# Performance work log

Measured on AMD Instinct MI355X. Metric: run time of the kernel, lower is better.

The kernel has to match this reference:

```python
import jax, jax.numpy as jnp
import numpy as np
import math

B, L, D = 32, 512, 256
H, DK, DV = 8, 32, 32
DFF = 2048
CONCAT = D * H * DV + D  # 65792


def setup_inputs() -> dict:
    key = jax.random.key(0)
    ks = jax.random.split(key, 12)
    s = 0.02
    return {
        "input_emb": jax.random.normal(ks[0], (B, L, D), jnp.float32),
        "emb_self_attn_mask": jax.random.bernoulli(ks[1], 0.1, (B, L, L)),
        "input_mask": jax.random.bernoulli(ks[2], 0.9, (B, L)).astype(jnp.int32),
        "W_Q": jax.random.normal(ks[3], (D, H * DK), jnp.float32) * s,
        "W_K": jax.random.normal(ks[4], (D, H * DK), jnp.float32) * s,
        "W_V": jax.random.normal(ks[5], (D, H * DV), jnp.float32) * s,
        "fc1_w": jax.random.normal(ks[6], (CONCAT, DFF), jnp.float32) * s,
        "fc1_b": jnp.zeros((DFF,), jnp.float32),
        "fc2_w": jax.random.normal(ks[7], (DFF, DFF), jnp.float32) * s,
        "fc2_b": jnp.zeros((DFF,), jnp.float32),
        "fc3_w": jax.random.normal(ks[8], (DFF, 1), jnp.float32) * s,
        "fc3_b": jnp.zeros((1,), jnp.float32),
    }


def reference(input_emb, emb_self_attn_mask, input_mask,
              W_Q, W_K, W_V, fc1_w, fc1_b, fc2_w, fc2_b, fc3_w, fc3_b):
    b, l, d = input_emb.shape
    # multi-head attention (hand-rolled SDPA)
    Q = (input_emb @ W_Q).reshape(b, l, H, DK).transpose(0, 2, 1, 3)  # [B,H,L,dk]
    K = (input_emb @ W_K).reshape(b, l, H, DK).transpose(0, 2, 1, 3)
    V = (input_emb @ W_V).reshape(b, l, H, DV).transpose(0, 2, 1, 3)
    scores = jnp.einsum("bhqd,bhkd->bhqk", Q, K) / math.sqrt(DK)
    scores = jnp.where(emb_self_attn_mask[:, None, :, :], -1e9, scores)
    attn = jax.nn.softmax(scores, axis=-1)
    context = jnp.einsum("bhqk,bhkd->bhqd", attn, V)
    context = context.transpose(0, 2, 1, 3).reshape(b, l, H * DV)  # [B,L,H*dv]
    # masked softmax pooling over the sequence dimension
    mask_exp = input_mask[:, :, None]  # [B,L,1]
    ctx_masked = jnp.where(mask_exp == 0, -1e9, context)
    weights = jax.nn.softmax(ctx_masked, axis=1)               # [B,L,H*dv]
    pooled = jnp.einsum("bld,blc->bdc", input_emb, weights)    # [B,D,H*dv]
    pooled_flat = pooled.reshape(b, -1)
    # masked mean pooling
    fmask = mask_exp.astype(input_emb.dtype)
    lengths = jnp.maximum(jnp.sum(input_mask, axis=1, keepdims=True), 1).astype(input_emb.dtype)
    avg_emb = jnp.sum(input_emb * fmask, axis=1) / lengths     # [B,D]
    x = jnp.concatenate([pooled_flat, avg_emb], axis=1)        # [B,CONCAT]
    h1 = jax.nn.relu(x @ fc1_w + fc1_b)
    h2 = jax.nn.relu(h1 @ fc2_w + fc2_b)
    out = h2 @ fc3_w + fc3_b                                    # [B,1]
    return (out, attn)
```

## Files before the change

kernel.cpp:

```cpp
#include <hip/hip_runtime.h>
#include <hip/hip_bf16.h>
#include <cstdint>

namespace {
constexpr int B  = 32;
constexpr int L  = 512;
constexpr int D  = 256;
constexpr int H  = 8;
constexpr int DV = 32;
constexpr int DFF = 2048;
constexpr int CONCAT = D * H * DV + D;
constexpr int BH = B * H;
}

typedef __attribute__((ext_vector_type(8))) short bf16x8;
typedef __attribute__((ext_vector_type(4))) float f32x4;

static __device__ __forceinline__ unsigned short f2bf_bits(float x) {
    __hip_bfloat16 h = __float2bfloat16(x);
    return *reinterpret_cast<unsigned short*>(&h);
}
static __device__ __forceinline__ float bf2f(short u) {
    unsigned int x = ((unsigned int)(unsigned short)u) << 16;
    union { unsigned int u; float f; } c; c.u = x; return c.f;
}
static __device__ __forceinline__ bf16x8 pack8(const float* v) {
    bf16x8 r;
#pragma unroll
    for (int j = 0; j < 8; ++j) r[j] = (short)f2bf_bits(v[j]);
    return r;
}

__global__ __launch_bounds__(256) void maskpack(const int* __restrict__ amask,
                                                unsigned int* __restrict__ mb) {
    const int t = threadIdx.x;
    const size_t gid = (size_t)blockIdx.x * 256 + t;
    int v = amask[gid];
    unsigned long long bal = __ballot(v != 0);
    if ((t & 63) == 0) *reinterpret_cast<unsigned long long*>(mb + (gid >> 5)) = bal;
}

__global__ __launch_bounds__(256) void transW(const float* __restrict__ WQ,
                                              const float* __restrict__ WK,
                                              const float* __restrict__ WV,
                                              __hip_bfloat16* __restrict__ WT) {
    const int mat = blockIdx.y;
    const int idx = blockIdx.x * 256 + threadIdx.x;
    const int n = idx >> 8, k = idx & 255;
    const float* W = (mat == 0) ? WQ : (mat == 1) ? WK : WV;
    WT[(size_t)mat * 65536 + idx] = __float2bfloat16(W[(size_t)k * 256 + n]);
}

__global__ __launch_bounds__(256) void embtrans(const float* __restrict__ emb,
                                                __hip_bfloat16* __restrict__ embB,
                                                __hip_bfloat16* __restrict__ embT) {
    const int lc = blockIdx.x;
    const int b  = blockIdx.y;
    const int t = threadIdx.x;
    __shared__ __hip_bfloat16 tile[64][264];
    const int l0 = lc * 64;
#pragma unroll 4
    for (int i = 0; i < 64; ++i) {
        float v = emb[((size_t)b * 512 + l0 + i) * 256 + t];
        __hip_bfloat16 hv = __float2bfloat16(v);
        embB[((size_t)b * 512 + l0 + i) * 256 + t] = hv;
        tile[i][t] = hv;
    }
    __syncthreads();
    __hip_bfloat16* dst = embT + ((size_t)b * 256 + t) * 512 + l0;
#pragma unroll
    for (int i0 = 0; i0 < 64; i0 += 8) {
        bf16x8 v;
#pragma unroll
        for (int j = 0; j < 8; ++j) v[j] = *reinterpret_cast<short*>(&tile[i0 + j][t]);
        *reinterpret_cast<bf16x8*>(dst + i0) = v;
    }
}

__global__ __launch_bounds__(256) void proj_mfma(const __hip_bfloat16* __restrict__ embB,
                                                 const __hip_bfloat16* __restrict__ WT,
                                                 __hip_bfloat16* __restrict__ Qb,
                                                 __hip_bfloat16* __restrict__ Kb,
                                                 __hip_bfloat16* __restrict__ Vt) {
    const int rb = blockIdx.x * 32;
    const int t = threadIdx.x;
    const int w = t >> 6, l = t & 63;
    const int lr = l & 15, lg = l >> 4;

    f32x4 accQ[2][4], accK[2][4], accV[2][4];
#pragma unroll
    for (int m = 0; m < 2; ++m)
#pragma unroll
        for (int n = 0; n < 4; ++n) {
            accQ[m][n] = (f32x4){0.f,0.f,0.f,0.f};
            accK[m][n] = (f32x4){0.f,0.f,0.f,0.f};
            accV[m][n] = (f32x4){0.f,0.f,0.f,0.f};
        }

    for (int kc = 0; kc < 8; ++kc) {
        const int k0 = kc * 32 + lg * 8;
        bf16x8 a0 = *reinterpret_cast<const bf16x8*>(embB + (size_t)(rb + lr) * 256 + k0);
        bf16x8 a1 = *reinterpret_cast<const bf16x8*>(embB + (size_t)(rb + 16 + lr) * 256 + k0);
#pragma unroll
        for (int nt = 0; nt < 4; ++nt) {
            const int col = w * 64 + nt * 16 + lr;
            bf16x8 bq = *reinterpret_cast<const bf16x8*>(WT + (size_t)col * 256 + k0);
            bf16x8 bk = *reinterpret_cast<const bf16x8*>(WT + 65536 + (size_t)col * 256 + k0);
            bf16x8 bv = *reinterpret_cast<const bf16x8*>(WT + 131072 + (size_t)col * 256 + k0);
            accQ[0][nt] = __builtin_amdgcn_mfma_f32_16x16x32_bf16(a0, bq, accQ[0][nt], 0, 0, 0);
            accQ[1][nt] = __builtin_amdgcn_mfma_f32_16x16x32_bf16(a1, bq, accQ[1][nt], 0, 0, 0);
            accK[0][nt] = __builtin_amdgcn_mfma_f32_16x16x32_bf16(a0, bk, accK[0][nt], 0, 0, 0);
            accK[1][nt] = __builtin_amdgcn_mfma_f32_16x16x32_bf16(a1, bk, accK[1][nt], 0, 0, 0);
            accV[0][nt] = __builtin_amdgcn_mfma_f32_16x16x32_bf16(a0, bv, accV[0][nt], 0, 0, 0);
            accV[1][nt] = __builtin_amdgcn_mfma_f32_16x16x32_bf16(a1, bv, accV[1][nt], 0, 0, 0);
        }
    }

    const int b = rb >> 9, l0 = rb & 511;
#pragma unroll
    for (int m = 0; m < 2; ++m)
#pragma unroll
        for (int nt = 0; nt < 4; ++nt) {
            const int n = w * 64 + nt * 16 + lr;
            const int h = n >> 5, d = n & 31;
            const int bh = b * 8 + h;
#pragma unroll
            for (int r = 0; r < 4; ++r) {
                const int ll = l0 + m * 16 + lg * 4 + r;
                Qb[((size_t)bh * 512 + ll) * 32 + d] = __float2bfloat16(accQ[m][nt][r]);
                Kb[((size_t)bh * 512 + ll) * 32 + d] = __float2bfloat16(accK[m][nt][r]);
                Vt[((size_t)bh * 32 + d) * 512 + ll] = __float2bfloat16(accV[m][nt][r]);
            }
        }
}

__global__ __launch_bounds__(256) void attn_mfma(const __hip_bfloat16* __restrict__ Q,
                                                 const __hip_bfloat16* __restrict__ K,
                                                 const __hip_bfloat16* __restrict__ Vt,
                                                 const unsigned int* __restrict__ mb,
                                                 float* __restrict__ attn_out,
                                                 float* __restrict__ ctx) {
    const int qt = blockIdx.x;
    const int bh = blockIdx.y;
    const int b = bh >> 3, h = bh & 7;
    const int t = threadIdx.x;
    const int w = t >> 6, l = t & 63;
    const int lr = l & 15, lg = l >> 4;
    const int q0 = qt * 16;

    __shared__ __hip_bfloat16 Pl[4][16][40];
    __shared__ float rmax[4][16];
    __shared__ float rsum[4][16];
    __shared__ float Ored[4][16][32];

    const float scale = 0.17677669529663687f;

    const bf16x8 aq = *reinterpret_cast<const bf16x8*>(Q + ((size_t)bh * L + q0 + lr) * 32 + lg * 8);
    const __hip_bfloat16* Kbase = K + (size_t)bh * L * 32;

    f32x4 sc[8];
#pragma unroll
    for (int kt = 0; kt < 8; ++kt) {
        bf16x8 bk = *reinterpret_cast<const bf16x8*>(
            Kbase + (size_t)((w * 8 + kt) * 16 + lr) * 32 + lg * 8);
        sc[kt] = __builtin_amdgcn_mfma_f32_16x16x32_bf16(aq, bk, (f32x4){0.f,0.f,0.f,0.f}, 0, 0, 0);
    }

    float tmp[4];
#pragma unroll
    for (int r = 0; r < 4; ++r) {
        const int q = q0 + lg * 4 + r;
        uint4 mw = *reinterpret_cast<const uint4*>(mb + ((size_t)b * L + q) * 16 + w * 4);
        const unsigned int wds[4] = {mw.x, mw.y, mw.z, mw.w};
        float m = -3.4e38f;
#pragma unroll
        for (int kt = 0; kt < 8; ++kt) {
            unsigned bit = (unsigned)lr + ((kt & 1) << 4);
            float s = ((wds[kt >> 1] >> bit) & 1u) ? -1e9f : sc[kt][r] * scale;
            sc[kt][r] = s;
            m = fmaxf(m, s);
        }
        m = fmaxf(m, __shfl_xor(m, 1));
        m = fmaxf(m, __shfl_xor(m, 2));
        m = fmaxf(m, __shfl_xor(m, 4));
        m = fmaxf(m, __shfl_xor(m, 8));
        tmp[r] = m;
    }
    if (lr == 0) {
#pragma unroll
        for (int r = 0; r < 4; ++r) rmax[w][lg * 4 + r] = tmp[r];
    }
    __syncthreads();

#pragma unroll
    for (int r = 0; r < 4; ++r) {
        const int row = lg * 4 + r;
        const float gm = fmaxf(fmaxf(rmax[0][row], rmax[1][row]),
                               fmaxf(rmax[2][row], rmax[3][row]));
        float sum = 0.f;
#pragma unroll
        for (int kt = 0; kt < 8; ++kt) {
            float e = __expf(sc[kt][r] - gm);
            sc[kt][r] = e;
            sum += e;
        }
        sum += __shfl_xor(sum, 1);
        sum += __shfl_xor(sum, 2);
        sum += __shfl_xor(sum, 4);
        sum += __shfl_xor(sum, 8);
        tmp[r] = sum;
    }
    if (lr == 0) {
#pragma unroll
        for (int r = 0; r < 4; ++r) rsum[w][lg * 4 + r] = tmp[r];
    }
    __syncthreads();

    const float my_ri = 1.f / (rsum[0][lr] + rsum[1][lr] + rsum[2][lr] + rsum[3][lr]);

    f32x4 acc0 = {0.f,0.f,0.f,0.f}, acc1 = {0.f,0.f,0.f,0.f};
    const __hip_bfloat16* Vb = Vt + (size_t)bh * 32 * L;
    float* aob = attn_out + ((size_t)bh * L + q0 + lr) * L + w * 128;
#pragma unroll
    for (int cc = 0; cc < 4; ++cc) {
#pragma unroll
        for (int r = 0; r < 4; ++r) {
            Pl[w][lg * 4 + r][lr]      = __float2bfloat16(sc[2*cc  ][r]);
            Pl[w][lg * 4 + r][16 + lr] = __float2bfloat16(sc[2*cc+1][r]);
        }
        __syncthreads();
        bf16x8 ap = *reinterpret_cast<const bf16x8*>(&Pl[w][lr][lg * 8]);
        float4 o0, o1;
        o0.x = bf2f(ap[0]) * my_ri; o0.y = bf2f(ap[1]) * my_ri;
        o0.z = bf2f(ap[2]) * my_ri; o0.w = bf2f(ap[3]) * my_ri;
        o1.x = bf2f(ap[4]) * my_ri; o1.y = bf2f(ap[5]) * my_ri;
        o1.z = bf2f(ap[6]) * my_ri; o1.w = bf2f(ap[7]) * my_ri;
        float* ao = aob + cc * 32 + lg * 8;
        *reinterpret_cast<float4*>(ao)     = o0;
        *reinterpret_cast<float4*>(ao + 4) = o1;
        bf16x8 bv0 = *reinterpret_cast<const bf16x8*>(Vb + (size_t)lr        * L + w * 128 + cc * 32 + lg * 8);
        bf16x8 bv1 = *reinterpret_cast<const bf16x8*>(Vb + (size_t)(16 + lr) * L + w * 128 + cc * 32 + lg * 8);
        acc0 = __builtin_amdgcn_mfma_f32_16x16x32_bf16(ap, bv0, acc0, 0, 0, 0);
        acc1 = __builtin_amdgcn_mfma_f32_16x16x32_bf16(ap, bv1, acc1, 0, 0, 0);
        __syncthreads();
    }

#pragma unroll
    for (int r = 0; r < 4; ++r) {
        Ored[w][lg * 4 + r][lr]      = acc0[r];
        Ored[w][lg * 4 + r][16 + lr] = acc1[r];
    }
    __syncthreads();
    for (int v = t; v < 512; v += 256) {
        const int row = v >> 5, col = v & 31;
        const float s = Ored[0][row][col] + Ored[1][row][col]
                      + Ored[2][row][col] + Ored[3][row][col];
        const float gs = rsum[0][row] + rsum[1][row] + rsum[2][row] + rsum[3][row];
        ctx[((size_t)b * L + q0 + row) * 256 + h * 32 + col] = s / gs;
    }
}

__global__ __launch_bounds__(256) void wts_kernel(const float* __restrict__ ctx,
                                                  const int* __restrict__ imask,
                                                  __hip_bfloat16* __restrict__ wtsT) {
    const int b = blockIdx.x >> 3;
    const int ct = blockIdx.x & 7;
    const int t = threadIdx.x;
    const int c = ct * 32 + (t & 31);
    const int g = t >> 5;
    __shared__ float rm[8][32];
    __shared__ float rs[8][32];
    __shared__ int mk[512];
    for (int p = t; p < 512; p += 256) mk[p] = imask[b * 512 + p];
    __syncthreads();

    float m = -3.4e38f;
    for (int ll = g; ll < 512; ll += 8) {
        float v = mk[ll] ? ctx[((size_t)b * 512 + ll) * 256 + c] : -1e9f;
        m = fmaxf(m, v);
    }
    rm[g][t & 31] = m;
    __syncthreads();
    float M = rm[0][t & 31];
#pragma unroll
    for (int q = 1; q < 8; ++q) M = fmaxf(M, rm[q][t & 31]);

    float sum = 0.f;
    for (int ll = g; ll < 512; ll += 8) {
        float v = mk[ll] ? ctx[((size_t)b * 512 + ll) * 256 + c] : -1e9f;
        sum += __expf(v - M);
    }
    rs[g][t & 31] = sum;
    __syncthreads();
    float S = 0.f;
#pragma unroll
    for (int q = 0; q < 8; ++q) S += rs[q][t & 31];
    const float rinv = 1.f / S;

    __hip_bfloat16* wrow = wtsT + ((size_t)b * 256 + c) * 512;
    for (int ll = g; ll < 512; ll += 8) {
        float v = mk[ll] ? ctx[((size_t)b * 512 + ll) * 256 + c] : -1e9f;
        wrow[ll] = __float2bfloat16(__expf(v - M) * rinv);
    }
}

__global__ __launch_bounds__(256) void pooled_mfma(const __hip_bfloat16* __restrict__ embT,
                                                   const __hip_bfloat16* __restrict__ wtsT,
                                                   __hip_bfloat16* __restrict__ xR) {
    const int ct = blockIdx.x, dt = blockIdx.y, b = blockIdx.z;
    const int t = threadIdx.x;
    const int w = t >> 6, l = t & 63;
    const int lr = l & 15, lg = l >> 4;
    const int wr = w >> 1, wc = w & 1;
    const int d0 = dt * 64 + wr * 32;
    const int c0 = ct * 64 + wc * 32;

    f32x4 acc[2][2];
#pragma unroll
    for (int m = 0; m < 2; ++m)
#pragma unroll
        for (int n = 0; n < 2; ++n) acc[m][n] = (f32x4){0.f,0.f,0.f,0.f};

    for (int lc = 0; lc < 16; ++lc) {
        const int lbase = lc * 32 + lg * 8;
        bf16x8 a[2], bb[2];
#pragma unroll
        for (int m = 0; m < 2; ++m)
            a[m] = *reinterpret_cast<const bf16x8*>(
                embT + ((size_t)b * 256 + d0 + m * 16 + lr) * 512 + lbase);
#pragma unroll
        for (int n = 0; n < 2; ++n)
            bb[n] = *reinterpret_cast<const bf16x8*>(
                wtsT + ((size_t)b * 256 + c0 + n * 16 + lr) * 512 + lbase);
#pragma unroll
        for (int m = 0; m < 2; ++m)
#pragma unroll
            for (int n = 0; n < 2; ++n)
                acc[m][n] = __builtin_amdgcn_mfma_f32_16x16x32_bf16(a[m], bb[n], acc[m][n], 0, 0, 0);
    }
#pragma unroll
    for (int m = 0; m < 2; ++m)
#pragma unroll
        for (int n = 0; n < 2; ++n)
#pragma unroll
            for (int r = 0; r < 4; ++r) {
                const int d = d0 + m * 16 + lg * 4 + r;
                const int c = c0 + n * 16 + lr;
                xR[(size_t)b * CONCAT + d * 256 + c] = __float2bfloat16(acc[m][n][r]);
            }
}

__global__ __launch_bounds__(256) void avg_part(const float* __restrict__ emb,
                                                const int* __restrict__ imask,
                                                float* __restrict__ avp,
                                                float* __restrict__ avc) {
    const int bg = blockIdx.x;
    const int b = bg >> 3, g = bg & 7;
    const int t = threadIdx.x;
    __shared__ int mk[64];
    if (t < 64) mk[t] = imask[b * L + g * 64 + t];
    __syncthreads();
    float s = 0.f;
#pragma unroll 4
    for (int i = 0; i < 64; ++i)
        if (mk[i]) s += emb[((size_t)b * L + g * 64 + i) * 256 + t];
    avp[(size_t)bg * 256 + t] = s;
    if (t == 0) {
        int c = 0;
#pragma unroll
        for (int i = 0; i < 64; ++i) c += (mk[i] != 0);
        avc[bg] = (float)c;
    }
}

__global__ __launch_bounds__(256) void avg_comb(const float* __restrict__ avp,
                                                const float* __restrict__ avc,
                                                __hip_bfloat16* __restrict__ xR) {
    const int b = blockIdx.x;
    const int t = threadIdx.x;
    float s = 0.f, c = 0.f;
#pragma unroll
    for (int g = 0; g < 8; ++g) {
        s += avp[(size_t)(b * 8 + g) * 256 + t];
        c += avc[b * 8 + g];
    }
    xR[(size_t)b * CONCAT + 65536 + t] = __float2bfloat16(s / fmaxf(c, 1.f));
}

template<int KSTEPS, int XSTRIDE, int CHUNK>
__global__ __launch_bounds__(256) void fc_mfma(const __hip_bfloat16* __restrict__ xR,
                                               const float* __restrict__ Wf,
                                               float* __restrict__ part,
                                               int kcbase) {
    const int bx = blockIdx.x;
    const int kc = blockIdx.y + kcbase;
    const int kbase = kc * CHUNK;
    const int t = threadIdx.x;
    const int w = t >> 6, l = t & 63;
    const int lr = l & 15, lg = l >> 4;
    const int col0 = bx * 256 + w * 64;

    f32x4 acc[2][4];
#pragma unroll
    for (int m = 0; m < 2; ++m)
#pragma unroll
        for (int n = 0; n < 4; ++n) acc[m][n] = (f32x4){0.f,0.f,0.f,0.f};

#pragma unroll 2
    for (int kt = 0; kt < KSTEPS; ++kt) {
        const int k = kbase + kt * 32 + lg * 8;
        bf16x8 a0 = *reinterpret_cast<const bf16x8*>(xR + (size_t)lr * XSTRIDE + k);
        bf16x8 a1 = *reinterpret_cast<const bf16x8*>(xR + (size_t)(16 + lr) * XSTRIDE + k);
#pragma unroll
        for (int nt = 0; nt < 4; ++nt) {
            const float* wp = Wf + (size_t)k * 2048 + col0 + nt * 16 + lr;
            float wv[8];
#pragma unroll
            for (int j = 0; j < 8; ++j) wv[j] = wp[(size_t)j * 2048];
            bf16x8 bw = pack8(wv);
            acc[0][nt] = __builtin_amdgcn_mfma_f32_16x16x32_bf16(a0, bw, acc[0][nt], 0, 0, 0);
            acc[1][nt] = __builtin_amdgcn_mfma_f32_16x16x32_bf16(a1, bw, acc[1][nt], 0, 0, 0);
        }
    }
    float* pp = part + (size_t)kc * 65536;
#pragma unroll
    for (int m = 0; m < 2; ++m)
#pragma unroll
        for (int nt = 0; nt < 4; ++nt)
#pragma unroll
            for (int r = 0; r < 4; ++r) {
                const int bb = m * 16 + lg * 4 + r;
                pp[(size_t)bb * 2048 + col0 + nt * 16 + lr] = acc[m][nt][r];
            }
}

__global__ __launch_bounds__(256) void fcreduce1(const float* __restrict__ part,
                                                 const float* __restrict__ bias,
                                                 __hip_bfloat16* __restrict__ outR) {
    const int t = threadIdx.x;
    const int o = blockIdx.x * 128 + (t & 127);
    const int half = t >> 7;
    __shared__ float red[128];
    float s = 0.f;
    if (half == 0) {
        for (int kc = 0; kc < 65; ++kc) s += part[(size_t)kc * 65536 + o];
    } else {
        for (int kc = 65; kc < 129; ++kc) s += part[(size_t)kc * 65536 + o];
    }
    if (half) red[t & 127] = s;
    __syncthreads();
    if (!half) {
        s += red[t];
        const int col = o & 2047;
        s = fmaxf(s + bias[col], 0.f);
        outR[o] = __float2bfloat16(s);
    }
}

__global__ __launch_bounds__(256) void fc23_kernel(const float* __restrict__ part2,
                                                   const float* __restrict__ b2,
                                                   const float* __restrict__ w3,
                                                   const float* __restrict__ b3,
                                                   float* __restrict__ out) {
    const int b = blockIdx.x;
    const int t = threadIdx.x;
    float s = 0.f;
    for (int c = t; c < DFF; c += 256) {
        float v = 0.f;
#pragma unroll
        for (int kc = 0; kc < 16; ++kc) v += part2[(size_t)kc * 65536 + b * 2048 + c];
        v = fmaxf(v + b2[c], 0.f);
        s += v * w3[c];
    }
#pragma unroll
    for (int o = 1; o < 64; o <<= 1) s += __shfl_xor(s, o);
    __shared__ float red[4];
    if ((t & 63) == 0) red[t >> 6] = s;
    __syncthreads();
    if (t == 0) out[b] = red[0] + red[1] + red[2] + red[3] + b3[0];
}

extern "C" void kernel_launch(void* const* d_in, const int* in_sizes, int n_in,
                              void* d_out, int out_size, void* d_ws, size_t ws_size,
                              hipStream_t stream) {
    const float* emb   = (const float*)d_in[0];
    const int*   amask = (const int*)d_in[1];
    const int*   imask = (const int*)d_in[2];
    const float* WQ    = (const float*)d_in[3];
    const float* WK    = (const float*)d_in[4];
    const float* WV    = (const float*)d_in[5];
    const float* fc1w  = (const float*)d_in[6];
    const float* fc1b  = (const float*)d_in[7];
    const float* fc2w  = (const float*)d_in[8];
    const float* fc2b  = (const float*)d_in[9];
    const float* fc3w  = (const float*)d_in[10];
    const float* fc3b  = (const float*)d_in[11];

    float* out_head = (float*)d_out;
    float* attn_out = out_head + 32;

    float* ws = (float*)d_ws;
    const size_t OFF_XR   = 0;
    const size_t OFF_Q    = OFF_XR + 1052672;
    const size_t OFF_K    = OFF_Q + 2097152;
    const size_t OFF_V    = OFF_K + 2097152;
    const size_t OFF_CTX  = OFF_V + 2097152;
    const size_t OFF_WTST = OFF_CTX + 4194304;
    const size_t OFF_P1   = OFF_WTST + 2097152;
    const size_t OFF_H1   = OFF_P1 + 8454144;
    const size_t OFF_P2   = OFF_H1 + 32768;
    const size_t OFF_MB   = OFF_P2 + 1048576;
    const size_t OFF_AVP  = OFF_MB + 262144;
    const size_t OFF_EMBB = OFF_AVP + 65792;
    const size_t OFF_EMBT = OFF_EMBB + 2097152;
    const size_t OFF_WT   = OFF_EMBT + 2097152;

    __hip_bfloat16* xR   = (__hip_bfloat16*)(ws + OFF_XR);
    __hip_bfloat16* Qb   = (__hip_bfloat16*)(ws + OFF_Q);
    __hip_bfloat16* Kb   = (__hip_bfloat16*)(ws + OFF_K);
    __hip_bfloat16* Vt   = (__hip_bfloat16*)(ws + OFF_V);
    float* ctx   = ws + OFF_CTX;
    __hip_bfloat16* wtsT = (__hip_bfloat16*)(ws + OFF_WTST);
    float* part1 = ws + OFF_P1;
    __hip_bfloat16* h1R  = (__hip_bfloat16*)(ws + OFF_H1);
    float* part2 = ws + OFF_P2;
    unsigned int* mbits = (unsigned int*)(ws + OFF_MB);
    float* avp   = ws + OFF_AVP;
    float* avc   = ws + OFF_AVP + 65536;
    __hip_bfloat16* embB = (__hip_bfloat16*)(ws + OFF_EMBB);
    __hip_bfloat16* embT = (__hip_bfloat16*)(ws + OFF_EMBT);
    __hip_bfloat16* WT   = (__hip_bfloat16*)(ws + OFF_WT);

    maskpack<<<dim3(32768), 256, 0, stream>>>(amask, mbits);
    transW<<<dim3(256, 3), 256, 0, stream>>>(WQ, WK, WV, WT);
    embtrans<<<dim3(8, B), 256, 0, stream>>>(emb, embB, embT);
    proj_mfma<<<dim3(512), 256, 0, stream>>>(embB, WT, Qb, Kb, Vt);
    attn_mfma<<<dim3(32, BH), 256, 0, stream>>>(Qb, Kb, Vt, mbits, attn_out, ctx);
    wts_kernel<<<dim3(B * 8), 256, 0, stream>>>(ctx, imask, wtsT);
    pooled_mfma<<<dim3(4, 4, B), 256, 0, stream>>>(embT, wtsT, xR);
    avg_part<<<dim3(B * 8), 256, 0, stream>>>(emb, imask, avp, avc);
    avg_comb<<<dim3(B), 256, 0, stream>>>(avp, avc, xR);

    fc_mfma<16, CONCAT, 512><<<dim3(8, 128), 256, 0, stream>>>(xR, fc1w, part1, 0);
    fc_mfma<8, CONCAT, 512><<<dim3(8, 1), 256, 0, stream>>>(xR, fc1w, part1, 128);
    fcreduce1<<<dim3(512), 256, 0, stream>>>(part1, fc1b, h1R);

    fc_mfma<4, DFF, 128><<<dim3(8, 16), 256, 0, stream>>>(h1R, fc2w, part2, 0);
    fc23_kernel<<<dim3(B), 256, 0, stream>>>(part2, fc2b, fc3w, fc3b, out_head);
}
```

Baseline: 424.6 us.

## Merge preprocessing kernels into one launch and read fp32 embeddings directly in projection

Combines mask packing, weight transposition, embedding transposition and masked-average partial sums into a single block-indexed prep kernel, removing three launches and the gaps between them. The bf16 row-major embedding copy is dropped: the projection kernel now loads fp32 embeddings and converts them to bf16 in registers. The embedding transpose tile shrinks to 32 rows so more blocks share that work. The cost is twice the global read bytes for the A operand in the projection, plus divergent block roles inside one grid.

```diff
diff --git a/kernel.cpp b/kernel.cpp
--- a/kernel.cpp
+++ b/kernel.cpp
@@ -31,53 +31,84 @@
     return r;
 }
 
-__global__ __launch_bounds__(256) void maskpack(const int* __restrict__ amask,
-                                                unsigned int* __restrict__ mb) {
-    const int t = threadIdx.x;
-    const size_t gid = (size_t)blockIdx.x * 256 + t;
-    int v = amask[gid];
-    unsigned long long bal = __ballot(v != 0);
-    if ((t & 63) == 0) *reinterpret_cast<unsigned long long*>(mb + (gid >> 5)) = bal;
-}
-
-__global__ __launch_bounds__(256) void transW(const float* __restrict__ WQ,
-                                              const float* __restrict__ WK,
-                                              const float* __restrict__ WV,
-                                              __hip_bfloat16* __restrict__ WT) {
-    const int mat = blockIdx.y;
-    const int idx = blockIdx.x * 256 + threadIdx.x;
-    const int n = idx >> 8, k = idx & 255;
-    const float* W = (mat == 0) ? WQ : (mat == 1) ? WK : WV;
-    WT[(size_t)mat * 65536 + idx] = __float2bfloat16(W[(size_t)k * 256 + n]);
-}
-
-__global__ __launch_bounds__(256) void embtrans(const float* __restrict__ emb,
-                                                __hip_bfloat16* __restrict__ embB,
-                                                __hip_bfloat16* __restrict__ embT) {
-    const int lc = blockIdx.x;
-    const int b  = blockIdx.y;
-    const int t = threadIdx.x;
-    __shared__ __hip_bfloat16 tile[64][264];
-    const int l0 = lc * 64;
+__global__ __launch_bounds__(256) void prep_kernel(const int* __restrict__ amask,
+                                                   unsigned int* __restrict__ mb,
+                                                   const float* __restrict__ WQ,
+                                                   const float* __restrict__ WK,
+                                                   const float* __restrict__ WV,
+                                                   __hip_bfloat16* __restrict__ WT,
+                                                   const float* __restrict__ emb,
+                                                   __hip_bfloat16* __restrict__ embT,
+                                                   const int* __restrict__ imask,
+                                                   float* __restrict__ avp,
+                                                   float* __restrict__ avc) {
+    __shared__ __hip_bfloat16 tile[32][264];
+    __shared__ int mk[64];
+    const int blk = blockIdx.x;
+    const int t = threadIdx.x;
+
+    if (blk < 32768) {
+        const size_t gid = (size_t)blk * 256 + t;
+        int v = amask[gid];
+        unsigned long long bal = __ballot(v != 0);
+        if ((t & 63) == 0) *reinterpret_cast<unsigned long long*>(mb + (gid >> 5)) = bal;
+    } else if (blk < 33536) {
+        const int e = blk - 32768;
+        const int mat = e >> 8, bx = e & 255;
+        const int idx = bx * 256 + t;
+        const int n = idx >> 8, k = idx & 255;
+        const float* W = (mat == 0) ? WQ : (mat == 1) ? WK : WV;
+        WT[(size_t)mat * 65536 + idx] = __float2bfloat16(W[(size_t)k * 256 + n]);
+    } else if (blk < 34048) {
+        const int e = blk - 33536;
+        const int lc = e & 15, b = e >> 4;
+        const int l0 = lc * 32;
 #pragma unroll 4
-    for (int i = 0; i < 64; ++i) {
-        float v = emb[((size_t)b * 512 + l0 + i) * 256 + t];
-        __hip_bfloat16 hv = __float2bfloat16(v);
-        embB[((size_t)b * 512 + l0 + i) * 256 + t] = hv;
-        tile[i][t] = hv;
-    }
-    __syncthreads();
-    __hip_bfloat16* dst = embT + ((size_t)b * 256 + t) * 512 + l0;
-#pragma unroll
-    for (int i0 = 0; i0 < 64; i0 += 8) {
-        bf16x8 v;
-#pragma unroll
-        for (int j = 0; j < 8; ++j) v[j] = *reinterpret_cast<short*>(&tile[i0 + j][t]);
-        *reinterpret_cast<bf16x8*>(dst + i0) = v;
-    }
-}
-
-__global__ __launch_bounds__(256) void proj_mfma(const __hip_bfloat16* __restrict__ embB,
+        for (int i = 0; i < 32; ++i)
+            tile[i][t] = __float2bfloat16(emb[((size_t)b * 512 + l0 + i) * 256 + t]);
+        __syncthreads();
+        __hip_bfloat16* dst = embT + ((size_t)b * 256 + t) * 512 + l0;
+#pragma unroll
+        for (int i0 = 0; i0 < 32; i0 += 8) {
+            bf16x8 v;
+#pragma unroll
+            for (int j = 0; j < 8; ++j) v[j] = *reinterpret_cast<short*>(&tile[i0 + j][t]);
+            *reinterpret_cast<bf16x8*>(dst + i0) = v;
+        }
+    } else {
+        const int bg = blk - 34048;
+        const int b = bg >> 3, g = bg & 7;
+        if (t < 64) mk[t] = imask[b * L + g * 64 + t];
+        __syncthreads();
+        float s = 0.f;
+#pragma unroll 4
+        for (int i = 0; i < 64; ++i)
+            if (mk[i]) s += emb[((size_t)b * L + g * 64 + i) * 256 + t];
+        avp[(size_t)bg * 256 + t] = s;
+        if (t == 0) {
+            int c = 0;
+#pragma unroll
+            for (int i = 0; i < 64; ++i) c += (mk[i] != 0);
+            avc[bg] = (float)c;
+        }
+    }
+}
+
+__global__ __launch_bounds__(256) void avg_comb(const float* __restrict__ avp,
+                                                const float* __restrict__ avc,
+                                                __hip_bfloat16* __restrict__ xR) {
+    const int b = blockIdx.x;
+    const int t = threadIdx.x;
+    float s = 0.f, c = 0.f;
+#pragma unroll
+    for (int g = 0; g < 8; ++g) {
+        s += avp[(size_t)(b * 8 + g) * 256 + t];
+        c += avc[b * 8 + g];
+    }
+    xR[(size_t)b * CONCAT + 65536 + t] = __float2bfloat16(s / fmaxf(c, 1.f));
+}
+
+__global__ __launch_bounds__(256) void proj_mfma(const float* __restrict__ emb,
                                                  const __hip_bfloat16* __restrict__ WT,
                                                  __hip_bfloat16* __restrict__ Qb,
                                                  __hip_bfloat16* __restrict__ Kb,
@@ -99,20 +130,27 @@
 
     for (int kc = 0; kc < 8; ++kc) {
         const int k0 = kc * 32 + lg * 8;
-        bf16x8 a0 = *reinterpret_cast<const bf16x8*>(embB + (size_t)(rb + lr) * 256 + k0);
-        bf16x8 a1 = *reinterpret_cast<const bf16x8*>(embB + (size_t)(rb + 16 + lr) * 256 + k0);
+        bf16x8 a[2];
+#pragma unroll
+        for (int m = 0; m < 2; ++m) {
+            const float* ap = emb + (size_t)(rb + m * 16 + lr) * 256 + k0;
+            float av[8];
+#pragma unroll
+            for (int j = 0; j < 8; ++j) av[j] = ap[j];
+            a[m] = pack8(av);
+        }
 #pragma unroll
         for (int nt = 0; nt < 4; ++nt) {
             const int col = w * 64 + nt * 16 + lr;
             bf16x8 bq = *reinterpret_cast<const bf16x8*>(WT + (size_t)col * 256 + k0);
             bf16x8 bk = *reinterpret_cast<const bf16x8*>(WT + 65536 + (size_t)col * 256 + k0);
             bf16x8 bv = *reinterpret_cast<const bf16x8*>(WT + 131072 + (size_t)col * 256 + k0);
-            accQ[0][nt] = __builtin_amdgcn_mfma_f32_16x16x32_bf16(a0, bq, accQ[0][nt], 0, 0, 0);
-            accQ[1][nt] = __builtin_amdgcn_mfma_f32_16x16x32_bf16(a1, bq, accQ[1][nt], 0, 0, 0);
-            accK[0][nt] = __builtin_amdgcn_mfma_f32_16x16x32_bf16(a0, bk, accK[0][nt], 0, 0, 0);
-            accK[1][nt] = __builtin_amdgcn_mfma_f32_16x16x32_bf16(a1, bk, accK[1][nt], 0, 0, 0);
-            accV[0][nt] = __builtin_amdgcn_mfma_f32_16x16x32_bf16(a0, bv, accV[0][nt], 0, 0, 0);
-            accV[1][nt] = __builtin_amdgcn_mfma_f32_16x16x32_bf16(a1, bv, accV[1][nt], 0, 0, 0);
+            accQ[0][nt] = __builtin_amdgcn_mfma_f32_16x16x32_bf16(a[0], bq, accQ[0][nt], 0, 0, 0);
+            accQ[1][nt] = __builtin_amdgcn_mfma_f32_16x16x32_bf16(a[1], bq, accQ[1][nt], 0, 0, 0);
+            accK[0][nt] = __builtin_amdgcn_mfma_f32_16x16x32_bf16(a[0], bk, accK[0][nt], 0, 0, 0);
+            accK[1][nt] = __builtin_amdgcn_mfma_f32_16x16x32_bf16(a[1], bk, accK[1][nt], 0, 0, 0);
+            accV[0][nt] = __builtin_amdgcn_mfma_f32_16x16x32_bf16(a[0], bv, accV[0][nt], 0, 0, 0);
+            accV[1][nt] = __builtin_amdgcn_mfma_f32_16x16x32_bf16(a[1], bv, accV[1][nt], 0, 0, 0);
         }
     }
 
@@ -350,43 +388,6 @@
             }
 }
 
-__global__ __launch_bounds__(256) void avg_part(const float* __restrict__ emb,
-                                                const int* __restrict__ imask,
-                                                float* __restrict__ avp,
-                                                float* __restrict__ avc) {
-    const int bg = blockIdx.x;
-    const int b = bg >> 3, g = bg & 7;
-    const int t = threadIdx.x;
-    __shared__ int mk[64];
-    if (t < 64) mk[t] = imask[b * L + g * 64 + t];
-    __syncthreads();
-    float s = 0.f;
-#pragma unroll 4
-    for (int i = 0; i < 64; ++i)
-        if (mk[i]) s += emb[((size_t)b * L + g * 64 + i) * 256 + t];
-    avp[(size_t)bg * 256 + t] = s;
-    if (t == 0) {
-        int c = 0;
-#pragma unroll
-        for (int i = 0; i < 64; ++i) c += (mk[i] != 0);
-        avc[bg] = (float)c;
-    }
-}
-
-__global__ __launch_bounds__(256) void avg_comb(const float* __restrict__ avp,
-                                                const float* __restrict__ avc,
-                                                __hip_bfloat16* __restrict__ xR) {
-    const int b = blockIdx.x;
-    const int t = threadIdx.x;
-    float s = 0.f, c = 0.f;
-#pragma unroll
-    for (int g = 0; g < 8; ++g) {
-        s += avp[(size_t)(b * 8 + g) * 256 + t];
-        c += avc[b * 8 + g];
-    }
-    xR[(size_t)b * CONCAT + 65536 + t] = __float2bfloat16(s / fmaxf(c, 1.f));
-}
-
 template<int KSTEPS, int XSTRIDE, int CHUNK>
 __global__ __launch_bounds__(256) void fc_mfma(const __hip_bfloat16* __restrict__ xR,
                                                const float* __restrict__ Wf,
@@ -511,8 +512,7 @@
     const size_t OFF_P2   = OFF_H1 + 32768;
     const size_t OFF_MB   = OFF_P2 + 1048576;
     const size_t OFF_AVP  = OFF_MB + 262144;
-    const size_t OFF_EMBB = OFF_AVP + 65792;
-    const size_t OFF_EMBT = OFF_EMBB + 2097152;
+    const size_t OFF_EMBT = OFF_AVP + 65792;
     const size_t OFF_WT   = OFF_EMBT + 2097152;
 
     __hip_bfloat16* xR   = (__hip_bfloat16*)(ws + OFF_XR);
@@ -527,18 +527,15 @@
     unsigned int* mbits = (unsigned int*)(ws + OFF_MB);
     float* avp   = ws + OFF_AVP;
     float* avc   = ws + OFF_AVP + 65536;
-    __hip_bfloat16* embB = (__hip_bfloat16*)(ws + OFF_EMBB);
     __hip_bfloat16* embT = (__hip_bfloat16*)(ws + OFF_EMBT);
     __hip_bfloat16* WT   = (__hip_bfloat16*)(ws + OFF_WT);
 
-    maskpack<<<dim3(32768), 256, 0, stream>>>(amask, mbits);
-    transW<<<dim3(256, 3), 256, 0, stream>>>(WQ, WK, WV, WT);
-    embtrans<<<dim3(8, B), 256, 0, stream>>>(emb, embB, embT);
-    proj_mfma<<<dim3(512), 256, 0, stream>>>(embB, WT, Qb, Kb, Vt);
+    prep_kernel<<<dim3(34304), 256, 0, stream>>>(amask, mbits, WQ, WK, WV, WT,
+                                                 emb, embT, imask, avp, avc);
+    proj_mfma<<<dim3(512), 256, 0, stream>>>(emb, WT, Qb, Kb, Vt);
     attn_mfma<<<dim3(32, BH), 256, 0, stream>>>(Qb, Kb, Vt, mbits, attn_out, ctx);
     wts_kernel<<<dim3(B * 8), 256, 0, stream>>>(ctx, imask, wtsT);
     pooled_mfma<<<dim3(4, 4, B), 256, 0, stream>>>(embT, wtsT, xR);
-    avg_part<<<dim3(B * 8), 256, 0, stream>>>(emb, imask, avp, avc);
     avg_comb<<<dim3(B), 256, 0, stream>>>(avp, avc, xR);
 
     fc_mfma<16, CONCAT, 512><<<dim3(8, 128), 256, 0, stream>>>(xR, fc1w, part1, 0);
```

Measured after the change: 411.4 us (median of 2 runs). -3.1%, faster.
